# Kernel tuning notes

Hardware: AMD Instinct MI355X
Metric: run time of the kernel (lower is better)

## Reference

```python
import jax, jax.numpy as jnp
import numpy as np

N = 10000
E = 160000
D_IN = 128
H = 1024
NUM_GRAPHS = 8
EPS = 1e-5


def setup_inputs() -> dict:
    key = jax.random.key(0)
    ks = jax.random.split(key, 24)
    x = jax.random.normal(ks[0], (N, D_IN), dtype=jnp.float32)
    edge_index = jax.random.randint(ks[1], (2, E), 0, N, dtype=jnp.int32)
    batch = jnp.sort(jax.random.randint(ks[2], (N,), 0, NUM_GRAPHS, dtype=jnp.int32))
    s = 0.02
    W1 = jax.random.normal(ks[3], (D_IN, H), dtype=jnp.float32) * s
    b1 = jnp.zeros((H,), jnp.float32)
    Wh = jax.random.normal(ks[4], (3, H, H), dtype=jnp.float32) * s
    bh = jnp.zeros((3, H), jnp.float32)
    ln_g = jnp.ones((4, H), jnp.float32)
    ln_b = jnp.zeros((4, H), jnp.float32)
    vW = jax.random.normal(ks[5], (6, H, H), dtype=jnp.float32) * s
    vb = jnp.zeros((6, H), jnp.float32)
    vWo = jax.random.normal(ks[6], (H, 1), dtype=jnp.float32) * s
    vbo = jnp.zeros((1,), jnp.float32)
    return {"x": x, "edge_index": edge_index, "batch": batch,
            "W1": W1, "b1": b1, "Wh": Wh, "bh": bh,
            "ln_g": ln_g, "ln_b": ln_b, "vW": vW, "vb": vb,
            "vWo": vWo, "vbo": vbo}


def _layer_norm(x, g, b):
    m = jnp.mean(x, axis=-1, keepdims=True)
    v = jnp.mean(jnp.square(x - m), axis=-1, keepdims=True)
    return (x - m) * jax.lax.rsqrt(v + EPS) * g + b


def reference(x, edge_index, batch, W1, b1, Wh, bh, ln_g, ln_b, vW, vb, vWo, vbo):
    # GCNConv: add self loops, symmetric normalization, x @ W, scatter-add at dst, + bias
    loops = jnp.arange(N, dtype=edge_index.dtype)
    src = jnp.concatenate([edge_index[0], loops])
    dst = jnp.concatenate([edge_index[1], loops])
    deg = jax.ops.segment_sum(jnp.ones_like(dst, dtype=x.dtype), dst, num_segments=N)
    dinv = jax.lax.rsqrt(jnp.maximum(deg, 1.0))
    norm = (dinv[src] * dinv[dst])[:, None]  # [E+N, 1]

    def gcn(h, W, b):
        h = h @ W                              # [N, H]
        msg = h[src] * norm                    # gather + scale [E+N, H]
        return jax.ops.segment_sum(msg, dst, num_segments=N) + b

    x1 = gcn(x, W1, b1)
    h = jax.nn.relu(_layer_norm(x1, ln_g[0], ln_b[0]))
    x2 = gcn(h, Wh[0], bh[0])
    h = jax.nn.relu(_layer_norm(x2 + x1, ln_g[1], ln_b[1]))
    x3 = gcn(h, Wh[1], bh[1])
    h = jax.nn.relu(_layer_norm(x3 + x1, ln_g[2], ln_b[2]))
    x4 = gcn(h, Wh[2], bh[2])
    node_embeddings = jax.nn.relu(_layer_norm(x4 + h, ln_g[3], ln_b[3]))

    # global mean pool per graph
    counts = jax.ops.segment_sum(jnp.ones((N,), x.dtype), batch, num_segments=NUM_GRAPHS)
    sums = jax.ops.segment_sum(node_embeddings, batch, num_segments=NUM_GRAPHS)
    graph_embedding = sums / jnp.maximum(counts, 1.0)[:, None]

    v = graph_embedding
    for i in range(6):
        v = jax.nn.relu(v @ vW[i] + vb[i])
    state_value = (v @ vWo + vbo).squeeze(-1)
    return node_embeddings, graph_embedding, state_value
```

## Files before the change

kernel.cpp:

```cpp
#include <hip/hip_runtime.h>
#include <stdint.h>

#define N_NODES 10000
#define E_EDGES 160000
#define DIN 128
#define H 1024
#define NUM_GRAPHS 8
#define LN_EPS 1e-5f

typedef unsigned short u16;
typedef __attribute__((ext_vector_type(8))) short short8;
typedef __attribute__((ext_vector_type(8))) unsigned short ushort8v;
typedef __attribute__((ext_vector_type(4))) float f32x4;

__device__ __forceinline__ float bf2f(u16 v) { return __uint_as_float(((unsigned)v) << 16); }
__device__ __forceinline__ u16 f2bf(float f) {
    unsigned u = __float_as_uint(f);
    u += 0x7fffu + ((u >> 16) & 1u);
    return (u16)(u >> 16);
}

__global__ void k_init(int* cnt, int* goff, float* __restrict__ gsum,
                       float* __restrict__ vbuf, const float* __restrict__ vb) {
    int i = blockIdx.x * 256 + threadIdx.x;
    if (i < N_NODES) cnt[i] = 0;
    if (i <= NUM_GRAPHS) goff[i] = 0;
    if (i < NUM_GRAPHS * H) gsum[i] = 0.f;
    if (i < 6 * H) {
        int il = i >> 10, j = i & (H - 1);
        float b = vb[il * H + j];
        float* base = vbuf + (size_t)(il + 1) * NUM_GRAPHS * H;
#pragma unroll
        for (int g = 0; g < NUM_GRAPHS; g++) base[g * H + j] = b;
    }
}

__global__ void k_setup(const int* __restrict__ dst, int* __restrict__ cnt,
                        const int* __restrict__ batch, int* __restrict__ goff,
                        const float* __restrict__ x, u16* __restrict__ xb) {
    int i = blockIdx.x * 256 + threadIdx.x;
    if (i < E_EDGES) atomicAdd(&cnt[dst[i]], 1);
    if (i < N_NODES) {
        int b0 = batch[i];
        int b1 = (i + 1 < N_NODES) ? batch[i + 1] : NUM_GRAPHS;
        for (int g = b0 + 1; g <= b1; g++) goff[g] = i + 1;
    }
    if (i < N_NODES * DIN) xb[i] = f2bf(x[i]);
}

__global__ __launch_bounds__(1024) void k_scan(const int* __restrict__ cnt, int* __restrict__ offs,
                                               int* __restrict__ cursor, float* __restrict__ dinv,
                                               int* __restrict__ perm) {
    __shared__ int wsum[16];
    __shared__ int carry_s;
    __shared__ int bins[256];
    __shared__ int binoff[256];
    int tid = threadIdx.x;
    int lane = tid & 63, wv = tid >> 6;
    if (tid == 0) carry_s = 0;
    if (tid < 256) bins[tid] = 0;
    __syncthreads();
    for (int base = 0; base < N_NODES; base += 1024) {
        int i = base + tid;
        int v = (i < N_NODES) ? cnt[i] : 0;
        if (i < N_NODES) atomicAdd(&bins[v < 255 ? v : 255], 1);
        int x = v;
#pragma unroll
        for (int off = 1; off < 64; off <<= 1) {
            int t = __shfl_up(x, off);
            if (lane >= off) x += t;
        }
        if (lane == 63) wsum[wv] = x;
        __syncthreads();
        int carry = carry_s;
        if (wv == 0) {
            int ws = (lane < 16) ? wsum[lane] : 0;
#pragma unroll
            for (int off = 1; off < 16; off <<= 1) {
                int t = __shfl_up(ws, off);
                if (lane >= off) ws += t;
            }
            if (lane < 16) wsum[lane] = ws;
        }
        __syncthreads();
        int wbase = (wv > 0) ? wsum[wv - 1] : 0;
        int incl = wbase + x;
        int excl = incl - v;
        if (i < N_NODES) {
            offs[i] = carry + excl;
            cursor[i] = carry + excl;
            dinv[i] = rsqrtf((float)(v + 1));
        }
        if (tid == 1023) carry_s = carry + incl;
        __syncthreads();
    }
    if (tid == 0) offs[N_NODES] = carry_s;
    if (tid < 256) binoff[tid] = bins[tid];
    __syncthreads();
    for (int off = 1; off < 256; off <<= 1) {
        int t = 0;
        if (tid < 256 && tid >= off) t = binoff[tid - off];
        __syncthreads();
        if (tid < 256) binoff[tid] += t;
        __syncthreads();
    }
    if (tid < 256) bins[tid] = binoff[tid] - bins[tid];
    __syncthreads();
    for (int base = 0; base < N_NODES; base += 1024) {
        int i = base + tid;
        if (i < N_NODES) {
            int v = cnt[i];
            v = v < 255 ? v : 255;
            int slot = atomicAdd(&bins[v], 1);
            perm[slot] = i;
        }
    }
}

__global__ void k_fill(const int* __restrict__ src, const int* __restrict__ dst,
                       int* __restrict__ cursor, int* __restrict__ csr_src) {
    int e = blockIdx.x * 256 + threadIdx.x;
    if (e < E_EDGES) {
        int d = dst[e];
        int slot = atomicAdd(&cursor[d], 1);
        csr_src[slot] = src[e];
    }
}

__global__ void k_wprep(const float* __restrict__ W1, const float* __restrict__ Wh,
                        u16* __restrict__ Wt1, u16* __restrict__ Wt3) {
    __shared__ float tile[32][33];
    int z = blockIdx.z;
    const float* src;
    u16* dst;
    int R;
    if (z == 0) {
        if (blockIdx.y * 32 >= DIN) return;
        src = W1; dst = Wt1; R = DIN;
    } else {
        src = Wh + (size_t)(z - 1) * H * H;
        dst = Wt3 + (size_t)(z - 1) * H * H;
        R = H;
    }
    const int C = H;
    int tx = threadIdx.x, ty = threadIdx.y;
    int x = blockIdx.x * 32 + tx;
#pragma unroll
    for (int i = 0; i < 32; i += 8) {
        int y = blockIdx.y * 32 + ty + i;
        tile[ty + i][tx] = (y < R && x < C) ? src[(size_t)y * C + x] : 0.f;
    }
    __syncthreads();
    int xo = blockIdx.y * 32 + tx;
#pragma unroll
    for (int i = 0; i < 32; i += 8) {
        int yo = blockIdx.x * 32 + ty + i;
        if (yo < C && xo < R) dst[(size_t)yo * R + xo] = f2bf(tile[tx][ty + i]);
    }
}

__global__ __launch_bounds__(64) void k_agg_x(const u16* __restrict__ xb, const float* __restrict__ dinv,
                                              const int* __restrict__ offs, const int* __restrict__ csr_src,
                                              u16* __restrict__ xa) {
    __shared__ float s_dv[64];
    __shared__ int s_id[64];
    int d = blockIdx.x;
    int tid = threadIdx.x;
    int c = tid * 2;
    float dd = dinv[d];
    float a0, a1;
    {
        unsigned v = *(const unsigned*)(xb + (size_t)d * DIN + c);
        a0 = dd * bf2f((u16)(v & 0xffffu));
        a1 = dd * bf2f((u16)(v >> 16));
    }
    int beg = offs[d], end = offs[d + 1];
    for (int chunk = beg; chunk < end; chunk += 64) {
        int nthis = end - chunk;
        if (nthis > 64) nthis = 64;
        int np = (nthis + 7) & ~7;
        __syncthreads();
        if (tid < nthis) {
            int s = csr_src[chunk + tid];
            s_id[tid] = s;
            s_dv[tid] = dinv[s];
        } else if (tid < np) {
            s_id[tid] = d;
            s_dv[tid] = 0.f;
        }
        __syncthreads();
        for (int i = 0; i < np; i += 8) {
            unsigned v[8];
            float e[8];
#pragma unroll
            for (int u = 0; u < 8; u++) {
                int s = s_id[i + u];
                e[u] = s_dv[i + u];
                v[u] = *(const unsigned*)(xb + (size_t)s * DIN + c);
            }
#pragma unroll
            for (int u = 0; u < 8; u++) {
                a0 += e[u] * bf2f((u16)(v[u] & 0xffffu));
                a1 += e[u] * bf2f((u16)(v[u] >> 16));
            }
        }
    }
    a0 *= dd;
    a1 *= dd;
    unsigned o = ((unsigned)f2bf(a1) << 16) | (unsigned)f2bf(a0);
    *(unsigned*)(xa + (size_t)d * DIN + c) = o;
}

__global__ __launch_bounds__(256) void k_agg_col(const u16* __restrict__ t, const float* __restrict__ dinv,
                                                 const int* __restrict__ offs, const int* __restrict__ csr_src,
                                                 const int* __restrict__ perm, u16* __restrict__ abuf) {
    int chunk = blockIdx.x & 7;
    int grp = threadIdx.x >> 4;
    int ln = threadIdx.x & 15;
    int d = perm[(blockIdx.x >> 3) * 16 + grp];
    int col = chunk * 128 + ln * 8;
    const u16* tc = t + col;
    float dd = dinv[d];
    float a[8];
    {
        ushort8v v = *(const ushort8v*)(tc + (size_t)d * H);
#pragma unroll
        for (int i = 0; i < 8; i++) a[i] = dd * bf2f(v[i]);
    }
    int e = offs[d], end = offs[d + 1];
    for (; e + 4 <= end; e += 4) {
        int s0 = csr_src[e], s1 = csr_src[e + 1], s2 = csr_src[e + 2], s3 = csr_src[e + 3];
        float w0 = dinv[s0], w1 = dinv[s1], w2 = dinv[s2], w3 = dinv[s3];
        ushort8v v0 = *(const ushort8v*)(tc + (size_t)s0 * H);
        ushort8v v1 = *(const ushort8v*)(tc + (size_t)s1 * H);
        ushort8v v2 = *(const ushort8v*)(tc + (size_t)s2 * H);
        ushort8v v3 = *(const ushort8v*)(tc + (size_t)s3 * H);
#pragma unroll
        for (int j = 0; j < 8; j++)
            a[j] += w0 * bf2f(v0[j]) + w1 * bf2f(v1[j]) + w2 * bf2f(v2[j]) + w3 * bf2f(v3[j]);
    }
    for (; e < end; e++) {
        int s0 = csr_src[e];
        float w0 = dinv[s0];
        ushort8v v0 = *(const ushort8v*)(tc + (size_t)s0 * H);
#pragma unroll
        for (int j = 0; j < 8; j++) a[j] += w0 * bf2f(v0[j]);
    }
    ushort8v o;
#pragma unroll
    for (int i = 0; i < 8; i++) o[i] = f2bf(dd * a[i]);
    __builtin_nontemporal_store(o, (ushort8v*)(abuf + (size_t)d * H + col));
}

template <int MODE>
__global__ __launch_bounds__(128) void k_ln(const u16* __restrict__ a, const u16* __restrict__ resid,
                                            const float* __restrict__ bias, const float* __restrict__ gamma,
                                            const float* __restrict__ beta,
                                            u16* __restrict__ out_bf, u16* __restrict__ out_pre,
                                            float* __restrict__ out_f32) {
    __shared__ float red1[2], red2[2];
    int d = blockIdx.x;
    int tid = threadIdx.x;
    int c = tid * 8;
    float x[8];
    {
        ushort8v v = *(const ushort8v*)(a + (size_t)d * H + c);
#pragma unroll
        for (int i = 0; i < 8; i++) x[i] = bf2f(v[i]) + bias[c + i];
    }
    if (MODE >= 1) {
        ushort8v r = *(const ushort8v*)(resid + (size_t)d * H + c);
#pragma unroll
        for (int i = 0; i < 8; i++) x[i] += bf2f(r[i]);
    }
    if (MODE == 0) {
        ushort8v p;
#pragma unroll
        for (int i = 0; i < 8; i++) p[i] = f2bf(x[i]);
        *(ushort8v*)(out_pre + (size_t)d * H + c) = p;
    }
    float s1 = 0.f, s2 = 0.f;
#pragma unroll
    for (int i = 0; i < 8; i++) { s1 += x[i]; s2 += x[i] * x[i]; }
#pragma unroll
    for (int off = 32; off > 0; off >>= 1) {
        s1 += __shfl_down(s1, off);
        s2 += __shfl_down(s2, off);
    }
    int lane = tid & 63, wv = tid >> 6;
    if (lane == 0) { red1[wv] = s1; red2[wv] = s2; }
    __syncthreads();
    float sum = red1[0] + red1[1];
    float ssq = red2[0] + red2[1];
    float mean = sum * (1.f / H);
    float var = fmaxf(ssq * (1.f / H) - mean * mean, 0.f);
    float inv = rsqrtf(var + LN_EPS);
    float y[8];
#pragma unroll
    for (int i = 0; i < 8; i++)
        y[i] = fmaxf((x[i] - mean) * inv * gamma[c + i] + beta[c + i], 0.f);
    if (MODE == 2) {
        float4 o0 = {y[0], y[1], y[2], y[3]};
        float4 o1 = {y[4], y[5], y[6], y[7]};
        *(float4*)(out_f32 + (size_t)d * H + c) = o0;
        *(float4*)(out_f32 + (size_t)d * H + c + 4) = o1;
    } else {
        ushort8v o;
#pragma unroll
        for (int i = 0; i < 8; i++) o[i] = f2bf(y[i]);
        *(ushort8v*)(out_bf + (size_t)d * H + c) = o;
    }
}

typedef __attribute__((address_space(1))) const unsigned int gas_u32;
typedef __attribute__((address_space(3))) unsigned int las_u32;
__device__ __forceinline__ void gld_lds16(const void* g, void* l) {
    __builtin_amdgcn_global_load_lds((gas_u32*)g, (las_u32*)l, 16, 0, 0);
}

__global__ __launch_bounds__(256) void k_gemm(const u16* __restrict__ A, const u16* __restrict__ B,
                                              u16* __restrict__ C, int M, int Nn, int K) {
    __shared__ __align__(16) u16 sA[2][128 * 32];
    __shared__ __align__(16) u16 sB[2][128 * 32];
    int mtiles = (M + 127) >> 7;
    int L = blockIdx.x;
    int cls = L & 7;
    int s = L >> 3;
    int nt = s & 7;
    int mt = (s >> 3) * 8 + cls;
    if (mt >= mtiles) return;
    int m0 = mt << 7;
    int n0 = nt << 7;

    int tid = threadIdx.x;
    int lane = tid & 63;
    int w = tid >> 6;
    int wm = w >> 1, wn = w & 1;

    f32x4 zero = {0.f, 0.f, 0.f, 0.f};
    f32x4 acc[4][4];
#pragma unroll
    for (int i = 0; i < 4; i++)
#pragma unroll
        for (int j = 0; j < 4; j++) acc[i][j] = zero;

    int srow = w * 32 + (lane >> 2);
    int scol = (((lane & 3) ^ ((lane >> 3) & 3))) * 8;

    auto STAGE = [&](int p, int k0) {
#pragma unroll
        for (int q = 0; q < 2; q++) {
            int rA = m0 + srow + q * 16;
            rA = rA < M ? rA : M - 1;
            gld_lds16(A + (size_t)rA * K + k0 + scol, sA[p] + w * 1024 + q * 512);
            gld_lds16(B + (size_t)(n0 + srow + q * 16) * K + k0 + scol, sB[p] + w * 1024 + q * 512);
        }
    };

    int NK = K >> 5;
    STAGE(0, 0);
    __syncthreads();

    int rchunk = ((lane >> 4) ^ ((lane >> 1) & 3)) * 8;
    int arow = (wm * 64 + (lane & 15)) * 32 + rchunk;
    int brow = (wn * 64 + (lane & 15)) * 32 + rchunk;

    for (int kt = 0; kt < NK; kt++) {
        int cur = kt & 1;
        if (kt + 1 < NK) STAGE(cur ^ 1, (kt + 1) << 5);

        short8 af[4], bv[4];
#pragma unroll
        for (int mi = 0; mi < 4; mi++)
            af[mi] = *(const short8*)(sA[cur] + arow + mi * 16 * 32);
#pragma unroll
        for (int ni = 0; ni < 4; ni++)
            bv[ni] = *(const short8*)(sB[cur] + brow + ni * 16 * 32);
#pragma unroll
        for (int mi = 0; mi < 4; mi++)
#pragma unroll
            for (int ni = 0; ni < 4; ni++)
                acc[mi][ni] = __builtin_amdgcn_mfma_f32_16x16x32_bf16(af[mi], bv[ni], acc[mi][ni], 0, 0, 0);

        __syncthreads();
    }

    int rbase = m0 + wm * 64 + (lane >> 4) * 4;
    int cbase = n0 + wn * 64 + (lane & 15);
#pragma unroll
    for (int mi = 0; mi < 4; mi++) {
#pragma unroll
        for (int r = 0; r < 4; r++) {
            int row = rbase + mi * 16 + r;
            if (row < M) {
#pragma unroll
                for (int ni = 0; ni < 4; ni++)
                    C[(size_t)row * Nn + cbase + ni * 16] = f2bf(acc[mi][ni][r]);
            }
        }
    }
}

#define PC_NODES 16
__global__ __launch_bounds__(256) void k_pool_acc(const float* __restrict__ ne, const int* __restrict__ batch,
                                                  float* __restrict__ gsum) {
    int c = blockIdx.x * 256 + threadIdx.x;
    int nbeg = blockIdx.y * PC_NODES;
    int nend = nbeg + PC_NODES;
    if (nend > N_NODES) nend = N_NODES;
    float acc = 0.f;
    int curg = batch[nbeg];
    for (int n = nbeg; n < nend; n++) {
        int g = batch[n];
        if (g != curg) {
            atomicAdd(&gsum[curg * H + c], acc);
            acc = 0.f;
            curg = g;
        }
        acc += ne[(size_t)n * H + c];
    }
    atomicAdd(&gsum[curg * H + c], acc);
}

__global__ __launch_bounds__(256) void k_pool_fin(const float* __restrict__ gsum, const int* __restrict__ goff,
                                                  float* __restrict__ v0, float* __restrict__ ge_out) {
    int g = blockIdx.y;
    int c = blockIdx.x * 256 + threadIdx.x;
    float cntf = (float)(goff[g + 1] - goff[g]);
    float m = gsum[g * H + c] / fmaxf(cntf, 1.f);
    v0[g * H + c] = m;
    ge_out[(size_t)g * H + c] = m;
}

template <bool RELU_IN>
__global__ __launch_bounds__(256) void k_mlp_acc(const float* __restrict__ vin, const float* __restrict__ W,
                                                 float* __restrict__ vout) {
    __shared__ float sk[64];
    int g = blockIdx.y;
    int j = blockIdx.x * 256 + threadIdx.x;
    int k0 = blockIdx.z * 64;
    if (threadIdx.x < 64) {
        float v = vin[g * H + k0 + threadIdx.x];
        sk[threadIdx.x] = RELU_IN ? fmaxf(v, 0.f) : v;
    }
    __syncthreads();
    float acc = 0.f;
#pragma unroll
    for (int k = 0; k < 64; k++) acc += sk[k] * W[(size_t)(k0 + k) * H + j];
    atomicAdd(&vout[g * H + j], acc);
}

__global__ void k_head(const float* __restrict__ vin, const float* __restrict__ Wo,
                       const float* __restrict__ bo, float* __restrict__ out) {
    int g = blockIdx.x;
    int tid = threadIdx.x;
    float s = 0.f;
    for (int k = tid; k < H; k += 256) s += fmaxf(vin[g * H + k], 0.f) * Wo[k];
#pragma unroll
    for (int off = 32; off > 0; off >>= 1) s += __shfl_down(s, off);
    __shared__ float p[4];
    if ((tid & 63) == 0) p[tid >> 6] = s;
    __syncthreads();
    if (tid == 0) out[g] = p[0] + p[1] + p[2] + p[3] + bo[0];
}

extern "C" void kernel_launch(void* const* d_in, const int* in_sizes, int n_in,
                              void* d_out, int out_size, void* d_ws, size_t ws_size,
                              hipStream_t stream) {
    const float* x = (const float*)d_in[0];
    const int* ei = (const int*)d_in[1];
    const int* batch = (const int*)d_in[2];
    const float* W1 = (const float*)d_in[3];
    const float* b1 = (const float*)d_in[4];
    const float* Wh = (const float*)d_in[5];
    const float* bh = (const float*)d_in[6];
    const float* ln_g = (const float*)d_in[7];
    const float* ln_b = (const float*)d_in[8];
    const float* vW = (const float*)d_in[9];
    const float* vb = (const float*)d_in[10];
    const float* vWo = (const float*)d_in[11];
    const float* vbo = (const float*)d_in[12];
    const int* esrc = ei;
    const int* edst = ei + E_EDGES;

    char* ws = (char*)d_ws;
    size_t off = 0;
    auto carve = [&](size_t bytes) -> char* {
        char* p = ws + off;
        off += (bytes + 255) & ~(size_t)255;
        return p;
    };
    float* dinv = (float*)carve(N_NODES * 4);
    int* cnt = (int*)carve(N_NODES * 4);
    int* offs = (int*)carve((N_NODES + 1) * 4);
    int* cursor = (int*)carve(N_NODES * 4);
    int* csr_src = (int*)carve(E_EDGES * 4);
    int* perm = (int*)carve(N_NODES * 4);
    int* goff = (int*)carve((NUM_GRAPHS + 1) * 4);
    float* gsum = (float*)carve(NUM_GRAPHS * H * 4);
    float* vbuf = (float*)carve((size_t)7 * NUM_GRAPHS * H * 4);
    u16* xb = (u16*)carve((size_t)N_NODES * DIN * 2);
    u16* xa = (u16*)carve((size_t)N_NODES * DIN * 2);
    u16* Wt1 = (u16*)carve((size_t)H * DIN * 2);
    u16* Wt3 = (u16*)carve((size_t)3 * H * H * 2);
    u16* tbuf = (u16*)carve((size_t)N_NODES * H * 2);
    u16* hbuf = (u16*)carve((size_t)N_NODES * H * 2);
    u16* x1buf = (u16*)carve((size_t)N_NODES * H * 2);
    u16* abuf = (u16*)carve((size_t)N_NODES * H * 2);

    float* out_ne = (float*)d_out;
    float* out_ge = out_ne + (size_t)N_NODES * H;
    float* out_sv = out_ge + (size_t)NUM_GRAPHS * H;

    k_init<<<(N_NODES + 255) / 256, 256, 0, stream>>>(cnt, goff, gsum, vbuf, vb);
    k_setup<<<(N_NODES * DIN + 255) / 256, 256, 0, stream>>>(edst, cnt, batch, goff, x, xb);
    k_scan<<<1, 1024, 0, stream>>>(cnt, offs, cursor, dinv, perm);
    k_fill<<<(E_EDGES + 255) / 256, 256, 0, stream>>>(esrc, edst, cursor, csr_src);
    k_wprep<<<dim3(H / 32, H / 32, 4), dim3(32, 8), 0, stream>>>(W1, Wh, Wt1, Wt3);

    int mtiles = (N_NODES + 127) / 128;
    int gemm_grid = 8 * 8 * ((mtiles + 7) / 8);
    int agg_grid = (N_NODES / 16) * 8;

    k_agg_x<<<N_NODES, 64, 0, stream>>>(xb, dinv, offs, csr_src, xa);
    k_gemm<<<gemm_grid, 256, 0, stream>>>(xa, Wt1, tbuf, N_NODES, H, DIN);
    k_ln<0><<<N_NODES, 128, 0, stream>>>(tbuf, nullptr, b1, ln_g, ln_b, hbuf, x1buf, nullptr);

    k_gemm<<<gemm_grid, 256, 0, stream>>>(hbuf, Wt3, tbuf, N_NODES, H, H);
    k_agg_col<<<agg_grid, 256, 0, stream>>>(tbuf, dinv, offs, csr_src, perm, abuf);
    k_ln<1><<<N_NODES, 128, 0, stream>>>(abuf, x1buf, bh, ln_g + H, ln_b + H, hbuf, nullptr, nullptr);

    k_gemm<<<gemm_grid, 256, 0, stream>>>(hbuf, Wt3 + (size_t)H * H, tbuf, N_NODES, H, H);
    k_agg_col<<<agg_grid, 256, 0, stream>>>(tbuf, dinv, offs, csr_src, perm, abuf);
    k_ln<1><<<N_NODES, 128, 0, stream>>>(abuf, x1buf, bh + H, ln_g + 2 * H, ln_b + 2 * H, hbuf, nullptr, nullptr);

    k_gemm<<<gemm_grid, 256, 0, stream>>>(hbuf, Wt3 + (size_t)2 * H * H, tbuf, N_NODES, H, H);
    k_agg_col<<<agg_grid, 256, 0, stream>>>(tbuf, dinv, offs, csr_src, perm, abuf);
    k_ln<2><<<N_NODES, 128, 0, stream>>>(abuf, hbuf, bh + 2 * H, ln_g + 3 * H, ln_b + 3 * H, nullptr, nullptr, out_ne);

    k_pool_acc<<<dim3(H / 256, (N_NODES + PC_NODES - 1) / PC_NODES), 256, 0, stream>>>(out_ne, batch, gsum);
    k_pool_fin<<<dim3(H / 256, NUM_GRAPHS), 256, 0, stream>>>(gsum, goff, vbuf, out_ge);

    dim3 mg(H / 256, NUM_GRAPHS, 16);
    k_mlp_acc<false><<<mg, 256, 0, stream>>>(vbuf, vW, vbuf + (size_t)1 * NUM_GRAPHS * H);
    for (int i = 1; i < 6; i++)
        k_mlp_acc<true><<<mg, 256, 0, stream>>>(vbuf + (size_t)i * NUM_GRAPHS * H, vW + (size_t)i * H * H,
                                                vbuf + (size_t)(i + 1) * NUM_GRAPHS * H);
    k_head<<<NUM_GRAPHS, 256, 0, stream>>>(vbuf + (size_t)6 * NUM_GRAPHS * H, vWo, vbo, out_sv);
}
```

Before: 433.9 us.

## Fuse bias, residual and LayerNorm statistics into aggregation; fold pool finalize into MLP

The column aggregation kernel now adds bias and residual, writes the pre-norm activation, and accumulates per-node sum and sum-of-squares into a small stats buffer with atomics. A lighter apply kernel then normalizes using those stats. This removes the residual re-read and the block reduction from the separate LayerNorm pass. The mean-pool finalize kernel is folded into the first MLP layer, saving one launch. The cost is extra atomics per node and a stats buffer that must be zeroed in the init kernel.

```diff
diff --git a/kernel.cpp b/kernel.cpp
--- a/kernel.cpp
+++ b/kernel.cpp
@@ -21,7 +21,8 @@
 }
 
 __global__ void k_init(int* cnt, int* goff, float* __restrict__ gsum,
-                       float* __restrict__ vbuf, const float* __restrict__ vb) {
+                       float* __restrict__ vbuf, const float* __restrict__ vb,
+                       float* __restrict__ sbufs) {
     int i = blockIdx.x * 256 + threadIdx.x;
     if (i < N_NODES) cnt[i] = 0;
     if (i <= NUM_GRAPHS) goff[i] = 0;
@@ -33,6 +34,7 @@
 #pragma unroll
         for (int g = 0; g < NUM_GRAPHS; g++) base[g * H + j] = b;
     }
+    for (int j = i; j < 3 * N_NODES * 2; j += 40 * 256) sbufs[j] = 0.f;
 }
 
 __global__ void k_setup(const int* __restrict__ dst, int* __restrict__ cnt,
@@ -211,9 +213,53 @@
     *(unsigned*)(xa + (size_t)d * DIN + c) = o;
 }
 
-__global__ __launch_bounds__(256) void k_agg_col(const u16* __restrict__ t, const float* __restrict__ dinv,
+__global__ __launch_bounds__(128) void k_ln1(const u16* __restrict__ t, const float* __restrict__ bias,
+                                             const float* __restrict__ gamma, const float* __restrict__ beta,
+                                             u16* __restrict__ out_bf, u16* __restrict__ out_pre) {
+    __shared__ float red1[2], red2[2];
+    int d = blockIdx.x;
+    int tid = threadIdx.x;
+    int c = tid * 8;
+    float x[8];
+    {
+        ushort8v v = *(const ushort8v*)(t + (size_t)d * H + c);
+#pragma unroll
+        for (int i = 0; i < 8; i++) x[i] = bf2f(v[i]) + bias[c + i];
+    }
+    {
+        ushort8v p;
+#pragma unroll
+        for (int i = 0; i < 8; i++) p[i] = f2bf(x[i]);
+        *(ushort8v*)(out_pre + (size_t)d * H + c) = p;
+    }
+    float s1 = 0.f, s2 = 0.f;
+#pragma unroll
+    for (int i = 0; i < 8; i++) { s1 += x[i]; s2 += x[i] * x[i]; }
+#pragma unroll
+    for (int off = 32; off > 0; off >>= 1) {
+        s1 += __shfl_down(s1, off);
+        s2 += __shfl_down(s2, off);
+    }
+    int lane = tid & 63, wv = tid >> 6;
+    if (lane == 0) { red1[wv] = s1; red2[wv] = s2; }
+    __syncthreads();
+    float sum = red1[0] + red1[1];
+    float ssq = red2[0] + red2[1];
+    float mean = sum * (1.f / H);
+    float var = fmaxf(ssq * (1.f / H) - mean * mean, 0.f);
+    float inv = rsqrtf(var + LN_EPS);
+    ushort8v o;
+#pragma unroll
+    for (int i = 0; i < 8; i++)
+        o[i] = f2bf(fmaxf((x[i] - mean) * inv * gamma[c + i] + beta[c + i], 0.f));
+    *(ushort8v*)(out_bf + (size_t)d * H + c) = o;
+}
+
+__global__ __launch_bounds__(256) void k_agg_col(const u16* __restrict__ t, const u16* __restrict__ resid,
+                                                 const float* __restrict__ bias, const float* __restrict__ dinv,
                                                  const int* __restrict__ offs, const int* __restrict__ csr_src,
-                                                 const int* __restrict__ perm, u16* __restrict__ abuf) {
+                                                 const int* __restrict__ perm, u16* __restrict__ abuf,
+                                                 float* __restrict__ sbuf) {
     int chunk = blockIdx.x & 7;
     int grp = threadIdx.x >> 4;
     int ln = threadIdx.x & 15;
@@ -246,69 +292,57 @@
 #pragma unroll
         for (int j = 0; j < 8; j++) a[j] += w0 * bf2f(v0[j]);
     }
+    ushort8v rv = *(const ushort8v*)(resid + (size_t)d * H + col);
     ushort8v o;
-#pragma unroll
-    for (int i = 0; i < 8; i++) o[i] = f2bf(dd * a[i]);
-    __builtin_nontemporal_store(o, (ushort8v*)(abuf + (size_t)d * H + col));
+    float s1 = 0.f, s2 = 0.f;
+#pragma unroll
+    for (int i = 0; i < 8; i++) {
+        float xi = dd * a[i] + bias[col + i] + bf2f(rv[i]);
+        o[i] = f2bf(xi);
+        float q = bf2f(o[i]);
+        s1 += q;
+        s2 += q * q;
+    }
+    *(ushort8v*)(abuf + (size_t)d * H + col) = o;
+#pragma unroll
+    for (int off = 1; off < 16; off <<= 1) {
+        s1 += __shfl_xor(s1, off);
+        s2 += __shfl_xor(s2, off);
+    }
+    if (ln == 0) {
+        atomicAdd(&sbuf[d * 2], s1);
+        atomicAdd(&sbuf[d * 2 + 1], s2);
+    }
 }
 
 template <int MODE>
-__global__ __launch_bounds__(128) void k_ln(const u16* __restrict__ a, const u16* __restrict__ resid,
-                                            const float* __restrict__ bias, const float* __restrict__ gamma,
-                                            const float* __restrict__ beta,
-                                            u16* __restrict__ out_bf, u16* __restrict__ out_pre,
-                                            float* __restrict__ out_f32) {
-    __shared__ float red1[2], red2[2];
-    int d = blockIdx.x;
-    int tid = threadIdx.x;
-    int c = tid * 8;
-    float x[8];
-    {
-        ushort8v v = *(const ushort8v*)(a + (size_t)d * H + c);
-#pragma unroll
-        for (int i = 0; i < 8; i++) x[i] = bf2f(v[i]) + bias[c + i];
-    }
-    if (MODE >= 1) {
-        ushort8v r = *(const ushort8v*)(resid + (size_t)d * H + c);
-#pragma unroll
-        for (int i = 0; i < 8; i++) x[i] += bf2f(r[i]);
-    }
-    if (MODE == 0) {
-        ushort8v p;
-#pragma unroll
-        for (int i = 0; i < 8; i++) p[i] = f2bf(x[i]);
-        *(ushort8v*)(out_pre + (size_t)d * H + c) = p;
-    }
-    float s1 = 0.f, s2 = 0.f;
-#pragma unroll
-    for (int i = 0; i < 8; i++) { s1 += x[i]; s2 += x[i] * x[i]; }
-#pragma unroll
-    for (int off = 32; off > 0; off >>= 1) {
-        s1 += __shfl_down(s1, off);
-        s2 += __shfl_down(s2, off);
-    }
-    int lane = tid & 63, wv = tid >> 6;
-    if (lane == 0) { red1[wv] = s1; red2[wv] = s2; }
-    __syncthreads();
-    float sum = red1[0] + red1[1];
-    float ssq = red2[0] + red2[1];
-    float mean = sum * (1.f / H);
-    float var = fmaxf(ssq * (1.f / H) - mean * mean, 0.f);
+__global__ __launch_bounds__(256) void k_ln_apply(const u16* __restrict__ abuf, const float* __restrict__ sbuf,
+                                                  const float* __restrict__ gamma, const float* __restrict__ beta,
+                                                  const int* __restrict__ perm,
+                                                  u16* __restrict__ out_bf, float* __restrict__ out_f32) {
+    int chunk = blockIdx.x & 7;
+    int grp = threadIdx.x >> 4;
+    int ln = threadIdx.x & 15;
+    int d = perm[(blockIdx.x >> 3) * 16 + grp];
+    int col = chunk * 128 + ln * 8;
+    float mean = sbuf[d * 2] * (1.f / H);
+    float var = fmaxf(sbuf[d * 2 + 1] * (1.f / H) - mean * mean, 0.f);
     float inv = rsqrtf(var + LN_EPS);
+    ushort8v v = *(const ushort8v*)(abuf + (size_t)d * H + col);
     float y[8];
 #pragma unroll
     for (int i = 0; i < 8; i++)
-        y[i] = fmaxf((x[i] - mean) * inv * gamma[c + i] + beta[c + i], 0.f);
+        y[i] = fmaxf((bf2f(v[i]) - mean) * inv * gamma[col + i] + beta[col + i], 0.f);
     if (MODE == 2) {
         float4 o0 = {y[0], y[1], y[2], y[3]};
         float4 o1 = {y[4], y[5], y[6], y[7]};
-        *(float4*)(out_f32 + (size_t)d * H + c) = o0;
-        *(float4*)(out_f32 + (size_t)d * H + c + 4) = o1;
+        *(float4*)(out_f32 + (size_t)d * H + col) = o0;
+        *(float4*)(out_f32 + (size_t)d * H + col + 4) = o1;
     } else {
         ushort8v o;
 #pragma unroll
         for (int i = 0; i < 8; i++) o[i] = f2bf(y[i]);
-        *(ushort8v*)(out_bf + (size_t)d * H + c) = o;
+        *(ushort8v*)(out_bf + (size_t)d * H + col) = o;
     }
 }
 
@@ -422,27 +456,30 @@
     atomicAdd(&gsum[curg * H + c], acc);
 }
 
-__global__ __launch_bounds__(256) void k_pool_fin(const float* __restrict__ gsum, const int* __restrict__ goff,
-                                                  float* __restrict__ v0, float* __restrict__ ge_out) {
+__global__ __launch_bounds__(256) void k_mlp0(const float* __restrict__ gsum, const int* __restrict__ goff,
+                                              const float* __restrict__ W, float* __restrict__ vout,
+                                              float* __restrict__ ge_out) {
+    __shared__ float sk[64];
     int g = blockIdx.y;
-    int c = blockIdx.x * 256 + threadIdx.x;
-    float cntf = (float)(goff[g + 1] - goff[g]);
-    float m = gsum[g * H + c] / fmaxf(cntf, 1.f);
-    v0[g * H + c] = m;
-    ge_out[(size_t)g * H + c] = m;
-}
-
-template <bool RELU_IN>
+    int j = blockIdx.x * 256 + threadIdx.x;
+    int k0 = blockIdx.z * 64;
+    float rinv = 1.f / fmaxf((float)(goff[g + 1] - goff[g]), 1.f);
+    if (threadIdx.x < 64) sk[threadIdx.x] = gsum[g * H + k0 + threadIdx.x] * rinv;
+    if (blockIdx.z == 0) ge_out[(size_t)g * H + j] = gsum[g * H + j] * rinv;
+    __syncthreads();
+    float acc = 0.f;
+#pragma unroll
+    for (int k = 0; k < 64; k++) acc += sk[k] * W[(size_t)(k0 + k) * H + j];
+    atomicAdd(&vout[g * H + j], acc);
+}
+
 __global__ __launch_bounds__(256) void k_mlp_acc(const float* __restrict__ vin, const float* __restrict__ W,
                                                  float* __restrict__ vout) {
     __shared__ float sk[64];
     int g = blockIdx.y;
     int j = blockIdx.x * 256 + threadIdx.x;
     int k0 = blockIdx.z * 64;
-    if (threadIdx.x < 64) {
-        float v = vin[g * H + k0 + threadIdx.x];
-        sk[threadIdx.x] = RELU_IN ? fmaxf(v, 0.f) : v;
-    }
+    if (threadIdx.x < 64) sk[threadIdx.x] = fmaxf(vin[g * H + k0 + threadIdx.x], 0.f);
     __syncthreads();
     float acc = 0.f;
 #pragma unroll
@@ -499,6 +536,7 @@
     int* goff = (int*)carve((NUM_GRAPHS + 1) * 4);
     float* gsum = (float*)carve(NUM_GRAPHS * H * 4);
     float* vbuf = (float*)carve((size_t)7 * NUM_GRAPHS * H * 4);
+    float* sbufs = (float*)carve((size_t)3 * N_NODES * 2 * 4);
     u16* xb = (u16*)carve((size_t)N_NODES * DIN * 2);
     u16* xa = (u16*)carve((size_t)N_NODES * DIN * 2);
     u16* Wt1 = (u16*)carve((size_t)H * DIN * 2);
@@ -512,7 +550,7 @@
     float* out_ge = out_ne + (size_t)N_NODES * H;
     float* out_sv = out_ge + (size_t)NUM_GRAPHS * H;
 
-    k_init<<<(N_NODES + 255) / 256, 256, 0, stream>>>(cnt, goff, gsum, vbuf, vb);
+    k_init<<<(N_NODES + 255) / 256, 256, 0, stream>>>(cnt, goff, gsum, vbuf, vb, sbufs);
     k_setup<<<(N_NODES * DIN + 255) / 256, 256, 0, stream>>>(edst, cnt, batch, goff, x, xb);
     k_scan<<<1, 1024, 0, stream>>>(cnt, offs, cursor, dinv, perm);
     k_fill<<<(E_EDGES + 255) / 256, 256, 0, stream>>>(esrc, edst, cursor, csr_src);
@@ -524,27 +562,26 @@
 
     k_agg_x<<<N_NODES, 64, 0, stream>>>(xb, dinv, offs, csr_src, xa);
     k_gemm<<<gemm_grid, 256, 0, stream>>>(xa, Wt1, tbuf, N_NODES, H, DIN);
-    k_ln<0><<<N_NODES, 128, 0, stream>>>(tbuf, nullptr, b1, ln_g, ln_b, hbuf, x1buf, nullptr);
+    k_ln1<<<N_NODES, 128, 0, stream>>>(tbuf, b1, ln_g, ln_b, hbuf, x1buf);
 
     k_gemm<<<gemm_grid, 256, 0, stream>>>(hbuf, Wt3, tbuf, N_NODES, H, H);
-    k_agg_col<<<agg_grid, 256, 0, stream>>>(tbuf, dinv, offs, csr_src, perm, abuf);
-    k_ln<1><<<N_NODES, 128, 0, stream>>>(abuf, x1buf, bh, ln_g + H, ln_b + H, hbuf, nullptr, nullptr);
+    k_agg_col<<<agg_grid, 256, 0, stream>>>(tbuf, x1buf, bh, dinv, offs, csr_src, perm, abuf, sbufs);
+    k_ln_apply<1><<<agg_grid, 256, 0, stream>>>(abuf, sbufs, ln_g + H, ln_b + H, perm, hbuf, nullptr);
 
     k_gemm<<<gemm_grid, 256, 0, stream>>>(hbuf, Wt3 + (size_t)H * H, tbuf, N_NODES, H, H);
-    k_agg_col<<<agg_grid, 256, 0, stream>>>(tbuf, dinv, offs, csr_src, perm, abuf);
-    k_ln<1><<<N_NODES, 128, 0, stream>>>(abuf, x1buf, bh + H, ln_g + 2 * H, ln_b + 2 * H, hbuf, nullptr, nullptr);
+    k_agg_col<<<agg_grid, 256, 0, stream>>>(tbuf, x1buf, bh + H, dinv, offs, csr_src, perm, abuf, sbufs + 2 * N_NODES);
+    k_ln_apply<1><<<agg_grid, 256, 0, stream>>>(abuf, sbufs + 2 * N_NODES, ln_g + 2 * H, ln_b + 2 * H, perm, hbuf, nullptr);
 
     k_gemm<<<gemm_grid, 256, 0, stream>>>(hbuf, Wt3 + (size_t)2 * H * H, tbuf, N_NODES, H, H);
-    k_agg_col<<<agg_grid, 256, 0, stream>>>(tbuf, dinv, offs, csr_src, perm, abuf);
-    k_ln<2><<<N_NODES, 128, 0, stream>>>(abuf, hbuf, bh + 2 * H, ln_g + 3 * H, ln_b + 3 * H, nullptr, nullptr, out_ne);
+    k_agg_col<<<agg_grid, 256, 0, stream>>>(tbuf, hbuf, bh + 2 * H, dinv, offs, csr_src, perm, abuf, sbufs + 4 * N_NODES);
+    k_ln_apply<2><<<agg_grid, 256, 0, stream>>>(abuf, sbufs + 4 * N_NODES, ln_g + 3 * H, ln_b + 3 * H, perm, nullptr, out_ne);
 
     k_pool_acc<<<dim3(H / 256, (N_NODES + PC_NODES - 1) / PC_NODES), 256, 0, stream>>>(out_ne, batch, gsum);
-    k_pool_fin<<<dim3(H / 256, NUM_GRAPHS), 256, 0, stream>>>(gsum, goff, vbuf, out_ge);
 
     dim3 mg(H / 256, NUM_GRAPHS, 16);
-    k_mlp_acc<false><<<mg, 256, 0, stream>>>(vbuf, vW, vbuf + (size_t)1 * NUM_GRAPHS * H);
+    k_mlp0<<<mg, 256, 0, stream>>>(gsum, goff, vW, vbuf + (size_t)1 * NUM_GRAPHS * H, out_ge);
     for (int i = 1; i < 6; i++)
-        k_mlp_acc<true><<<mg, 256, 0, stream>>>(vbuf + (size_t)i * NUM_GRAPHS * H, vW + (size_t)i * H * H,
-                                                vbuf + (size_t)(i + 1) * NUM_GRAPHS * H);
+        k_mlp_acc<<<mg, 256, 0, stream>>>(vbuf + (size_t)i * NUM_GRAPHS * H, vW + (size_t)i * H * H,
+                                          vbuf + (size_t)(i + 1) * NUM_GRAPHS * H);
     k_head<<<NUM_GRAPHS, 256, 0, stream>>>(vbuf + (size_t)6 * NUM_GRAPHS * H, vWo, vbo, out_sv);
 }
```

New measurement: 443.3 us. 1.02x slower.

## Fuse mean-pool and value MLP into one cooperative kernel with grid syncs

Applied to the files above, without the earlier changes.

Replaces the atomic pool-accumulate, pool-finalize, six MLP layer kernels and head kernel with a single cooperative kernel of 64 blocks. Each block owns 16 output columns, computes the per-graph means from the contiguous graph ranges and then runs all six layers with grid.sync between them, keeping activations in ping-pong buffers and staging inputs in shared memory. This removes about nine launches and the atomics and buffer initialisation. In exchange only 64 blocks stream the 4 MB per-layer weights, and the pooling reads 40 MB from few blocks, so bandwidth utilisation may drop.

```diff
diff --git a/kernel.cpp b/kernel.cpp
--- a/kernel.cpp
+++ b/kernel.cpp
@@ -1,5 +1,8 @@
 #include <hip/hip_runtime.h>
+#include <hip/hip_cooperative_groups.h>
 #include <stdint.h>
+
+namespace cg = cooperative_groups;
 
 #define N_NODES 10000
 #define E_EDGES 160000
@@ -20,19 +23,10 @@
     return (u16)(u >> 16);
 }
 
-__global__ void k_init(int* cnt, int* goff, float* __restrict__ gsum,
-                       float* __restrict__ vbuf, const float* __restrict__ vb) {
+__global__ void k_init(int* cnt, int* goff) {
     int i = blockIdx.x * 256 + threadIdx.x;
     if (i < N_NODES) cnt[i] = 0;
     if (i <= NUM_GRAPHS) goff[i] = 0;
-    if (i < NUM_GRAPHS * H) gsum[i] = 0.f;
-    if (i < 6 * H) {
-        int il = i >> 10, j = i & (H - 1);
-        float b = vb[il * H + j];
-        float* base = vbuf + (size_t)(il + 1) * NUM_GRAPHS * H;
-#pragma unroll
-        for (int g = 0; g < NUM_GRAPHS; g++) base[g * H + j] = b;
-    }
 }
 
 __global__ void k_setup(const int* __restrict__ dst, int* __restrict__ cnt,
@@ -401,67 +395,74 @@
     }
 }
 
-#define PC_NODES 16
-__global__ __launch_bounds__(256) void k_pool_acc(const float* __restrict__ ne, const int* __restrict__ batch,
-                                                  float* __restrict__ gsum) {
-    int c = blockIdx.x * 256 + threadIdx.x;
-    int nbeg = blockIdx.y * PC_NODES;
-    int nend = nbeg + PC_NODES;
-    if (nend > N_NODES) nend = N_NODES;
-    float acc = 0.f;
-    int curg = batch[nbeg];
-    for (int n = nbeg; n < nend; n++) {
-        int g = batch[n];
-        if (g != curg) {
-            atomicAdd(&gsum[curg * H + c], acc);
-            acc = 0.f;
-            curg = g;
-        }
-        acc += ne[(size_t)n * H + c];
-    }
-    atomicAdd(&gsum[curg * H + c], acc);
-}
-
-__global__ __launch_bounds__(256) void k_pool_fin(const float* __restrict__ gsum, const int* __restrict__ goff,
-                                                  float* __restrict__ v0, float* __restrict__ ge_out) {
-    int g = blockIdx.y;
-    int c = blockIdx.x * 256 + threadIdx.x;
-    float cntf = (float)(goff[g + 1] - goff[g]);
-    float m = gsum[g * H + c] / fmaxf(cntf, 1.f);
-    v0[g * H + c] = m;
-    ge_out[(size_t)g * H + c] = m;
-}
-
-template <bool RELU_IN>
-__global__ __launch_bounds__(256) void k_mlp_acc(const float* __restrict__ vin, const float* __restrict__ W,
-                                                 float* __restrict__ vout) {
-    __shared__ float sk[64];
-    int g = blockIdx.y;
-    int j = blockIdx.x * 256 + threadIdx.x;
-    int k0 = blockIdx.z * 64;
-    if (threadIdx.x < 64) {
-        float v = vin[g * H + k0 + threadIdx.x];
-        sk[threadIdx.x] = RELU_IN ? fmaxf(v, 0.f) : v;
-    }
-    __syncthreads();
-    float acc = 0.f;
-#pragma unroll
-    for (int k = 0; k < 64; k++) acc += sk[k] * W[(size_t)(k0 + k) * H + j];
-    atomicAdd(&vout[g * H + j], acc);
-}
-
-__global__ void k_head(const float* __restrict__ vin, const float* __restrict__ Wo,
-                       const float* __restrict__ bo, float* __restrict__ out) {
-    int g = blockIdx.x;
+__global__ __launch_bounds__(256) void k_mlp_all(const float* __restrict__ ne, const int* __restrict__ goff,
+                                                 const float* __restrict__ vW, const float* __restrict__ vb,
+                                                 const float* __restrict__ vWo, const float* __restrict__ vbo,
+                                                 float* __restrict__ ge_out, float* __restrict__ act0,
+                                                 float* __restrict__ act1, float* __restrict__ out_sv) {
+    cg::grid_group grid = cg::this_grid();
+    __shared__ float red[256];
+    __shared__ float in_s[8 * 1032];
+    int cc = blockIdx.x;
     int tid = threadIdx.x;
-    float s = 0.f;
-    for (int k = tid; k < H; k += 256) s += fmaxf(vin[g * H + k], 0.f) * Wo[k];
-#pragma unroll
-    for (int off = 32; off > 0; off >>= 1) s += __shfl_down(s, off);
-    __shared__ float p[4];
-    if ((tid & 63) == 0) p[tid >> 6] = s;
-    __syncthreads();
-    if (tid == 0) out[g] = p[0] + p[1] + p[2] + p[3] + bo[0];
+    int jl = tid & 15;
+    int gg = (tid >> 4) & 7;
+    int q = tid >> 7;
+    int col = cc * 16 + jl;
+
+    {
+        int nbeg = goff[gg], nend = goff[gg + 1];
+        float s = 0.f;
+        for (int r = nbeg + q; r < nend; r += 2) s += ne[(size_t)r * H + col];
+        red[tid] = s;
+        __syncthreads();
+        if (tid < 128) {
+            int g2 = tid >> 4, j2 = tid & 15;
+            int cnt = goff[g2 + 1] - goff[g2];
+            float m = (red[tid] + red[tid + 128]) / fmaxf((float)cnt, 1.f);
+            ge_out[(size_t)g2 * H + cc * 16 + j2] = m;
+            act0[(size_t)g2 * H + cc * 16 + j2] = m;
+        }
+    }
+    grid.sync();
+
+    const float* in = act0;
+    float* out = act1;
+#pragma unroll 1
+    for (int l = 0; l < 6; l++) {
+        for (int idx = tid; idx < 8 * H; idx += 256)
+            in_s[(idx >> 10) * 1032 + (idx & (H - 1))] = in[idx];
+        __syncthreads();
+        const float* Wl = vW + (size_t)l * H * H;
+        float acc = 0.f;
+        int kb = q * 512;
+        const float* ip = in_s + gg * 1032 + kb;
+        const float* wp = Wl + (size_t)kb * H + col;
+#pragma unroll 8
+        for (int k = 0; k < 512; k++) acc += ip[k] * wp[(size_t)k * H];
+        __syncthreads();
+        red[tid] = acc;
+        __syncthreads();
+        if (tid < 128) {
+            int g2 = tid >> 4, j2 = tid & 15;
+            float o = red[tid] + red[tid + 128] + vb[l * H + cc * 16 + j2];
+            out[(size_t)g2 * H + cc * 16 + j2] = fmaxf(o, 0.f);
+        }
+        grid.sync();
+        const float* tmp = in; in = out; out = (float*)tmp;
+    }
+    if (cc < NUM_GRAPHS) {
+        float p = 0.f;
+        for (int k = tid; k < H; k += 256) p += in[(size_t)cc * H + k] * vWo[k];
+        red[tid] = p;
+        __syncthreads();
+        if (tid < 64) {
+            float t4 = red[tid] + red[tid + 64] + red[tid + 128] + red[tid + 192];
+#pragma unroll
+            for (int off = 32; off > 0; off >>= 1) t4 += __shfl_down(t4, off);
+            if (tid == 0) out_sv[cc] = t4 + vbo[0];
+        }
+    }
 }
 
 extern "C" void kernel_launch(void* const* d_in, const int* in_sizes, int n_in,
@@ -497,8 +498,8 @@
     int* csr_src = (int*)carve(E_EDGES * 4);
     int* perm = (int*)carve(N_NODES * 4);
     int* goff = (int*)carve((NUM_GRAPHS + 1) * 4);
-    float* gsum = (float*)carve(NUM_GRAPHS * H * 4);
-    float* vbuf = (float*)carve((size_t)7 * NUM_GRAPHS * H * 4);
+    float* act0 = (float*)carve((size_t)NUM_GRAPHS * H * 4);
+    float* act1 = (float*)carve((size_t)NUM_GRAPHS * H * 4);
     u16* xb = (u16*)carve((size_t)N_NODES * DIN * 2);
     u16* xa = (u16*)carve((size_t)N_NODES * DIN * 2);
     u16* Wt1 = (u16*)carve((size_t)H * DIN * 2);
@@ -512,7 +513,7 @@
     float* out_ge = out_ne + (size_t)N_NODES * H;
     float* out_sv = out_ge + (size_t)NUM_GRAPHS * H;
 
-    k_init<<<(N_NODES + 255) / 256, 256, 0, stream>>>(cnt, goff, gsum, vbuf, vb);
+    k_init<<<(N_NODES + 255) / 256, 256, 0, stream>>>(cnt, goff);
     k_setup<<<(N_NODES * DIN + 255) / 256, 256, 0, stream>>>(edst, cnt, batch, goff, x, xb);
     k_scan<<<1, 1024, 0, stream>>>(cnt, offs, cursor, dinv, perm);
     k_fill<<<(E_EDGES + 255) / 256, 256, 0, stream>>>(esrc, edst, cursor, csr_src);
@@ -538,13 +539,8 @@
     k_agg_col<<<agg_grid, 256, 0, stream>>>(tbuf, dinv, offs, csr_src, perm, abuf);
     k_ln<2><<<N_NODES, 128, 0, stream>>>(abuf, hbuf, bh + 2 * H, ln_g + 3 * H, ln_b + 3 * H, nullptr, nullptr, out_ne);
 
-    k_pool_acc<<<dim3(H / 256, (N_NODES + PC_NODES - 1) / PC_NODES), 256, 0, stream>>>(out_ne, batch, gsum);
-    k_pool_fin<<<dim3(H / 256, NUM_GRAPHS), 256, 0, stream>>>(gsum, goff, vbuf, out_ge);
-
-    dim3 mg(H / 256, NUM_GRAPHS, 16);
-    k_mlp_acc<false><<<mg, 256, 0, stream>>>(vbuf, vW, vbuf + (size_t)1 * NUM_GRAPHS * H);
-    for (int i = 1; i < 6; i++)
-        k_mlp_acc<true><<<mg, 256, 0, stream>>>(vbuf + (size_t)i * NUM_GRAPHS * H, vW + (size_t)i * H * H,
-                                                vbuf + (size_t)(i + 1) * NUM_GRAPHS * H);
-    k_head<<<NUM_GRAPHS, 256, 0, stream>>>(vbuf + (size_t)6 * NUM_GRAPHS * H, vWo, vbo, out_sv);
-}
+    const float* ne_p = out_ne;
+    void* args[] = {(void*)&ne_p, (void*)&goff, (void*)&vW, (void*)&vb, (void*)&vWo, (void*)&vbo,
+                    (void*)&out_ge, (void*)&act0, (void*)&act1, (void*)&out_sv};
+    hipLaunchCooperativeKernel((void*)k_mlp_all, dim3(64), dim3(256), args, 0, stream);
+}
```

New measurement: 891.3 us. +105.4%, slower.
